# Performance work log

Measured on AMD Instinct MI355X. Metric: run time of the kernel, lower is better.

Reference implementation:

```python
import jax, jax.numpy as jnp
import numpy as np

N, D, E, K, L, NF, VOCAB = 100000, 128, 600000, 3, 3, 9, 100
BN_EPS = 1e-5
S = 0.05


def setup_inputs() -> dict:
    key = jax.random.key(0)
    ks = jax.random.split(key, 8)
    return {
        "x": jax.random.randint(ks[0], (N, NF), 0, VOCAB),
        "k_edges": jax.random.randint(ks[1], (K, 2, E), 0, N),
        "emb_tables": jax.random.normal(ks[2], (NF, VOCAB, D), jnp.float32) * S,
        "W1": jax.random.normal(ks[3], (L, D, 2 * D), jnp.float32) * S,
        "b1": jnp.zeros((L, 2 * D), jnp.float32),
        "g1": jnp.ones((L, 2 * D), jnp.float32),
        "be1": jnp.zeros((L, 2 * D), jnp.float32),
        "W2": jax.random.normal(ks[4], (L, 2 * D, D), jnp.float32) * S,
        "b2": jnp.zeros((L, D), jnp.float32),
        "eps": jnp.zeros((L,), jnp.float32),
        "alpha": jnp.zeros((L, K), jnp.float32),
        "bn_g": jnp.ones((L, D), jnp.float32),
        "bn_b": jnp.zeros((L, D), jnp.float32),
    }


def _bn(h, g, b):
    # training-mode BatchNorm1d over the node (batch) axis
    mu = h.mean(axis=0)
    var = h.var(axis=0)
    return (h - mu) * jax.lax.rsqrt(var + BN_EPS) * g + b


def _gin(h, src, dst, eps_l, W1_l, b1_l, g1_l, be1_l, W2_l, b2_l):
    # NodeGINConv (train_eps): mlp((1+eps)*x + sum_{j->i} x_j)
    agg = jax.ops.segment_sum(h[src], dst, num_segments=N)  # [N, D]
    z = (1.0 + eps_l) * h + agg
    z = jax.nn.relu(_bn(z @ W1_l + b1_l, g1_l, be1_l))  # [N, 2D]
    return z @ W2_l + b2_l  # [N, D]


def reference(x, k_edges, emb_tables, W1, b1, g1, be1, W2, b2, eps, alpha, bn_g, bn_b):
    # AtomEncoder: sum of per-feature embedding lookups -> [N, D]
    h = jnp.take_along_axis(
        emb_tables.transpose(1, 0, 2),  # [VOCAB, NF, D]
        x.T[..., None].transpose(1, 0, 2) * 0 + 0,  # placeholder avoided below
        axis=0,
    ) if False else emb_tables[jnp.arange(NF)[None, :], x].sum(axis=1)
    for l in range(L):
        # one shared wrapped GIN conv applied to each of the K relational edge sets
        msgs = jax.vmap(
            lambda e: _gin(h, e[0], e[1], eps[l], W1[l], b1[l], g1[l], be1[l], W2[l], b2[l])
        )(k_edges)  # [K, N, D]
        a = jax.nn.softmax(alpha[l])  # [K]
        h = jnp.einsum('knd,k->nd', msgs, a)
        h = jax.nn.relu(_bn(h, bn_g[l], bn_b[l]))  # dropout p=0 / eval -> identity
    return h
```

## Files before the change

kernel.cpp:

```cpp
#include <hip/hip_runtime.h>

#define NV     100000
#define DD     128
#define D2     256
#define EE     600000
#define KK     3
#define LL     3
#define NFEAT  9
#define VOCABS 100

#define NBKT   196
#define BCAP   8192

typedef __attribute__((ext_vector_type(8))) short short8;
typedef __attribute__((ext_vector_type(4))) float f32x4;
typedef __attribute__((ext_vector_type(2))) float f32x2;
typedef __attribute__((ext_vector_type(4))) unsigned int uint4v;

#define PA      0

#define ZS(k)  ((k)*512)
#define ZQ(k)  ((k)*512 + 256)
#define HSUM   1536
#define HSQ    1664

#define HB_OFF   ((size_t)0)
#define ZIN_OFF  ((size_t)25700000)
#define HNB_OFF  ((size_t)102500000)
#define O_BASE   ((size_t)128100000)


__device__ __forceinline__ unsigned short f2bf(float f) {
    union { float f; unsigned int u; } v; v.f = f;
    return (unsigned short)((v.u + 0x7FFFu + ((v.u >> 16) & 1u)) >> 16);
}
__device__ __forceinline__ float bf2f(unsigned short u) {
    union { unsigned int u; float f; } v; v.u = ((unsigned int)u) << 16;
    return v.f;
}
__device__ __forceinline__ f32x2 up2(unsigned int v) {
    union { unsigned int u[2]; f32x2 f; } w;
    w.u[0] = v << 16;
    w.u[1] = v & 0xFFFF0000u;
    return w.f;
}

__global__ void k_embed(const int* __restrict__ x, const float* __restrict__ emb,
                        unsigned short* __restrict__ hb) {
    int id = blockIdx.x*256 + threadIdx.x;
    int n = id >> 5, q = id & 31;
    if (n >= NV) {
        if (n < NV + 8) *(unsigned long long*)(hb + (size_t)n*DD + q*4) = 0ull;
        return;
    }
    const int* xr = x + n*NFEAT;
    f32x4 acc = {0.f,0.f,0.f,0.f};
    #pragma unroll
    for (int f = 0; f < NFEAT; ++f) {
        int idx = xr[f];
        acc += *(const f32x4*)(emb + ((size_t)(f*VOCABS + idx)*DD + q*4));
    }
    unsigned short pk[4];
    pk[0] = f2bf(acc[0]); pk[1] = f2bf(acc[1]); pk[2] = f2bf(acc[2]); pk[3] = f2bf(acc[3]);
    *(unsigned long long*)(hb + (size_t)n*DD + q*4) = *(unsigned long long*)pk;
}

__global__ void kA_bin(const int* __restrict__ ke, int* __restrict__ cursor,
                       uint2* __restrict__ pairs) {
    __shared__ int hist[NBKT], excl[NBKT], ofs[NBKT], gbase[NBKT];
    __shared__ int sc[256];
    __shared__ uint2 buf[4096];
    const int rel = blockIdx.y, t = threadIdx.x;
    const int e0 = blockIdx.x * 4096;
    const int cnt = min(4096, EE - e0);
    const int* srcA = ke + (size_t)(rel*2)*EE + e0;
    const int* dstA = ke + (size_t)(rel*2+1)*EE + e0;
    if (t < NBKT) hist[t] = 0;
    __syncthreads();
    for (int i = t; i < cnt; i += 256) atomicAdd(&hist[dstA[i] >> 9], 1);
    __syncthreads();
    const int hv = (t < NBKT) ? hist[t] : 0;
    sc[t] = hv;
    for (int off = 1; off < 256; off <<= 1) {
        __syncthreads();
        int v = (t >= off) ? sc[t-off] : 0;
        __syncthreads();
        sc[t] += v;
    }
    __syncthreads();
    if (t < NBKT) {
        excl[t] = sc[t] - hv;
        ofs[t]  = sc[t] - hv;
        if (hv > 0) gbase[t] = atomicAdd(&cursor[rel*NBKT + t], hv);
    }
    __syncthreads();
    for (int i = t; i < cnt; i += 256) {
        unsigned int s = (unsigned int)srcA[i], d = (unsigned int)dstA[i];
        int p = atomicAdd(&ofs[d >> 9], 1);
        uint2 u; u.x = s; u.y = d;
        buf[p] = u;
    }
    __syncthreads();
    for (int i = t; i < cnt; i += 256) {
        uint2 u = buf[i];
        int b = (int)(u.y >> 9);
        int pos = gbase[b] + (i - excl[b]);
        if (pos < BCAP) pairs[(size_t)(rel*NBKT + b)*BCAP + pos] = u;
    }
}

__global__ void kB_scan(const int* __restrict__ cursor, int* __restrict__ ebase) {
    __shared__ int sc[256];
    const int t = threadIdx.x;
    for (int rel = 0; rel < KK; ++rel) {
        int hv = (t < NBKT) ? min(cursor[rel*NBKT + t], BCAP) : 0;
        sc[t] = hv;
        for (int off = 1; off < 256; off <<= 1) {
            __syncthreads();
            int v = (t >= off) ? sc[t-off] : 0;
            __syncthreads();
            sc[t] += v;
        }
        __syncthreads();
        if (t < NBKT) ebase[rel*NBKT + t] = sc[t] - hv;
        __syncthreads();
    }
}

__global__ void kB_fill(const uint2* __restrict__ pairs, const int* __restrict__ cursor,
                        const int* __restrict__ ebase, int* __restrict__ rp,
                        int* __restrict__ col) {
    __shared__ int h2[512], excl[512], cur[512], sc[256];
    const int b = blockIdx.x, rel = blockIdx.y, t = threadIdx.x;
    const int lo = b * 512;
    const int cnt = min(cursor[rel*NBKT + b], BCAP);
    const int base = ebase[rel*NBKT + b];
    const uint2* P = pairs + (size_t)(rel*NBKT + b)*BCAP;
    h2[t] = 0; h2[t+256] = 0; cur[t] = 0; cur[t+256] = 0;
    __syncthreads();
    for (int i = t; i < cnt; i += 256) atomicAdd(&h2[(int)P[i].y - lo], 1);
    __syncthreads();
    const int a0 = h2[2*t], a1 = h2[2*t+1];
    sc[t] = a0 + a1;
    for (int off = 1; off < 256; off <<= 1) {
        __syncthreads();
        int v = (t >= off) ? sc[t-off] : 0;
        __syncthreads();
        sc[t] += v;
    }
    __syncthreads();
    const int e2 = sc[t] - (a0 + a1);
    excl[2*t] = e2; excl[2*t+1] = e2 + a0;
    __syncthreads();
    for (int tt = t; tt < 512; tt += 256) {
        int n = lo + tt;
        if (n <= NV) rp[(size_t)rel*(NV+1) + n] = base + excl[tt];
    }
    for (int i = t; i < cnt; i += 256) {
        uint2 u = P[i];
        int r = (int)u.y - lo;
        int p = atomicAdd(&cur[r], 1);
        col[(size_t)rel*EE + base + excl[r] + p] = (int)u.x;
    }
}

__global__ void k_prep(const float* __restrict__ W1, const float* __restrict__ W2,
                       const float* __restrict__ alpha, const int l,
                       unsigned short* __restrict__ w1f, unsigned short* __restrict__ w2f,
                       float* __restrict__ params) {
    int id = blockIdx.x*256 + threadIdx.x;
    if (id == 0) {
        float a0 = alpha[l*KK+0], a1 = alpha[l*KK+1], a2 = alpha[l*KK+2];
        float m = fmaxf(a0, fmaxf(a1, a2));
        float e0 = expf(a0-m), e1 = expf(a1-m), e2 = expf(a2-m);
        float inv = 1.f/(e0+e1+e2);
        params[PA+0] = e0*inv; params[PA+1] = e1*inv; params[PA+2] = e2*inv;
    }
    if (id < 4096) {
        int kt = id >> 10, nt = (id >> 6) & 15, lane = id & 63;
        int r = lane & 15, g = lane >> 4;
        const float* Wl = W1 + (size_t)l*DD*D2;
        #pragma unroll
        for (int e = 0; e < 8; ++e) {
            int kk = kt*32 + g*8 + e, c = nt*16 + r;
            w1f[(size_t)id*8 + e] = f2bf(Wl[(size_t)kk*D2 + c]);
        }
    } else if (id < 8192) {
        int id2 = id - 4096;
        int kt = id2 >> 9, nt = (id2 >> 6) & 7, lane = id2 & 63;
        int r = lane & 15, g = lane >> 4;
        const float* Wl = W2 + (size_t)l*D2*DD;
        #pragma unroll
        for (int e = 0; e < 8; ++e) {
            int kk = kt*32 + g*8 + e, c = nt*16 + r;
            w2f[(size_t)id2*8 + e] = f2bf(Wl[(size_t)kk*DD + c]);
        }
    }
}

__global__ void k_gather3(const unsigned short* __restrict__ hb, const int* __restrict__ rp,
                          const int* __restrict__ col, const float* __restrict__ epsp,
                          unsigned short* __restrict__ zin) {
    int gid = blockIdx.x*256 + threadIdx.x;
    int n0 = gid >> 6;
    if (n0 >= NV) return;
    const int n = __builtin_amdgcn_readfirstlane(n0);
    const int lane = threadIdx.x & 63;
    const int q = lane >> 4, r = lane & 15;
    const int r16 = r << 4;
    const char* hbase = (const char*)hb;
    const float epsv = 1.0f + epsp[0];
    const uint4v sv = *(const uint4v*)(hbase + (((unsigned)n << 8) + r16));
    int b0[KK], dg[KK], cv[KK];
    #pragma unroll
    for (int k = 0; k < KK; ++k) {
        int a = rp[k*(NV+1) + n];
        int b = rp[k*(NV+1) + n + 1];
        b0[k] = a; dg[k] = b - a;
        cv[k] = (lane < dg[k]) ? col[(size_t)k*EE + a + lane] : NV;
    }
    f32x2 acc[KK][4];
    #pragma unroll
    for (int k = 0; k < KK; ++k)
        #pragma unroll
        for (int c = 0; c < 4; ++c) acc[k][c] = (f32x2){0.f, 0.f};
    #pragma unroll
    for (int k = 0; k < KK; ++k) {
        const int dc = min(dg[k], 64);
        for (int base = 0; base < dc; base += 8) {
            int s0 = __shfl(cv[k], base + q);
            int s1 = __shfl(cv[k], base + q + 4);
            uint4v v0 = *(const uint4v*)(hbase + (((unsigned)s0 << 8) + r16));
            uint4v v1 = *(const uint4v*)(hbase + (((unsigned)s1 << 8) + r16));
            #pragma unroll
            for (int c = 0; c < 4; ++c) {
                acc[k][c] += up2(v0[c]);
                acc[k][c] += up2(v1[c]);
            }
        }
        for (int j = b0[k] + 64 + q; j < b0[k] + dg[k]; j += 4) {
            int s0 = col[(size_t)k*EE + j];
            uint4v v0 = *(const uint4v*)(hbase + (((unsigned)s0 << 8) + r16));
            #pragma unroll
            for (int c = 0; c < 4; ++c) acc[k][c] += up2(v0[c]);
        }
    }
    #pragma unroll
    for (int k = 0; k < KK; ++k) {
        #pragma unroll
        for (int c = 0; c < 4; ++c) {
            acc[k][c][0] += __shfl_xor(acc[k][c][0], 16);
            acc[k][c][1] += __shfl_xor(acc[k][c][1], 16);
            acc[k][c][0] += __shfl_xor(acc[k][c][0], 32);
            acc[k][c][1] += __shfl_xor(acc[k][c][1], 32);
        }
    }
    if (q == 0) {
        const unsigned dsto = (((unsigned)n >> 4) << 12) + ((unsigned)r << 8)
                            + (((unsigned)n & 15u) << 4);
        #pragma unroll
        for (int k = 0; k < KK; ++k) {
            uint4v pk;
            #pragma unroll
            for (int c = 0; c < 4; ++c) {
                f32x2 s2 = up2(sv[c]);
                float lo = acc[k][c][0] + epsv * s2[0];
                float hi = acc[k][c][1] + epsv * s2[1];
                unsigned int pko;
                asm("v_cvt_pk_bf16_f32 %0, %1, %2" : "=v"(pko) : "v"(lo), "v"(hi));
                pk[c] = pko;
            }
            *(uint4v*)((char*)zin + (size_t)k*NV*256 + dsto) = pk;
        }
    }
}

__launch_bounds__(256, 2)
__global__ void k_stats3(const unsigned short* __restrict__ zin,
                         const unsigned short* __restrict__ w1f,
                         float* __restrict__ statsL) {
    __shared__ __align__(16) unsigned short bfr1[32768];
    __shared__ float scf[1024];
    const int t = threadIdx.x;
    const int krel = blockIdx.y;
    const char* zk = (const char*)zin + (size_t)krel*NV*256;
    float* zsum = statsL + ZS(krel);
    float* zsq  = statsL + ZQ(krel);
    for (int i = t; i < 4096; i += 256)
        *(uint4v*)(bfr1 + i*8) = *(const uint4v*)(w1f + i*8);
    const int lane = t & 63, w = t >> 6;
    const int r_ = lane & 15, g = lane >> 4;
    const int rt = w & 1, ch = w >> 1;
    __syncthreads();
    float ssum[8] = {0,0,0,0,0,0,0,0};
    float ssq[8]  = {0,0,0,0,0,0,0,0};
    for (int tile = blockIdx.x; tile < NV/32; tile += gridDim.x) {
        short8 af[4];
        #pragma unroll
        for (int kt = 0; kt < 4; ++kt)
            af[kt] = *(const short8*)(zk + (size_t)(tile*2 + rt)*4096 + kt*1024 + lane*16);
        #pragma unroll
        for (int ct = 0; ct < 8; ++ct) {
            const int ntg = ch*8 + ct;
            f32x4 c = {0.f,0.f,0.f,0.f};
            #pragma unroll
            for (int kt = 0; kt < 4; ++kt) {
                short8 b = *(const short8*)(bfr1 + ((size_t)((kt*16 + ntg)*64 + lane))*8);
                c = __builtin_amdgcn_mfma_f32_16x16x32_bf16(af[kt], b, c, 0, 0, 0);
            }
            float s = c[0]+c[1]+c[2]+c[3];
            float q = c[0]*c[0]+c[1]*c[1]+c[2]*c[2]+c[3]*c[3];
            s += __shfl_xor(s, 16); q += __shfl_xor(q, 16);
            s += __shfl_xor(s, 32); q += __shfl_xor(q, 32);
            ssum[ct] += s; ssq[ct] += q;
        }
    }
    if (g == 0) {
        #pragma unroll
        for (int ct = 0; ct < 8; ++ct) {
            const int colc = (ch*8 + ct)*16 + r_;
            scf[rt*256 + colc]       = ssum[ct];
            scf[512 + rt*256 + colc] = ssq[ct];
        }
    }
    __syncthreads();
    atomicAdd(zsum + t, scf[t]       + scf[256 + t]);
    atomicAdd(zsq  + t, scf[512 + t] + scf[768 + t]);
}

__launch_bounds__(512, 2)
__global__ void k_gemm2f(const unsigned short* __restrict__ zin,
                         const unsigned short* __restrict__ w1f,
                         const unsigned short* __restrict__ w2f,
                         const float* __restrict__ g1l, const float* __restrict__ be1l,
                         const float* __restrict__ params,
                         float* __restrict__ statsL,
                         unsigned short* __restrict__ hnb) {
    __shared__ __align__(16) unsigned short bfr1[32768];
    __shared__ __align__(16) unsigned short bfr2[32768];
    __shared__ __align__(16) unsigned char yt[16384];
    const int t = threadIdx.x;
    for (int i = t; i < 4096; i += 512)
        *(uint4v*)(bfr1 + i*8) = *(const uint4v*)(w1f + i*8);
    for (int i = t; i < 4096; i += 512)
        *(uint4v*)(bfr2 + i*8) = *(const uint4v*)(w2f + i*8);
    const int lane = t & 63, w = t >> 6;
    const int r_ = lane & 15, g = lane >> 4;
    const int rt = w & 1, ch = w >> 1;
    const int arow = rt*16 + r_;
    float pa1[KK][4], pb1[KK][4];
    #pragma unroll
    for (int k = 0; k < KK; ++k) {
        const float ak = params[PA + k];
        #pragma unroll
        for (int ct = 0; ct < 4; ++ct) {
            const int colc = (ch*4 + ct)*16 + r_;
            float mu  = statsL[ZS(k) + colc] * (1.0f/NV);
            float var = statsL[ZQ(k) + colc] * (1.0f/NV) - mu*mu;
            float A = g1l[colc] * rsqrtf(var + 1e-5f);
            pa1[k][ct] = ak * A;
            pb1[k][ct] = ak * (be1l[colc] - mu*A);
        }
    }
    __syncthreads();
    float ssum[2] = {0,0}, ssq[2] = {0,0};
    for (int tile = blockIdx.x; tile < NV/32; tile += gridDim.x) {
        const int row0 = tile*32;
        f32x4 y[4];
        #pragma unroll
        for (int ct = 0; ct < 4; ++ct) y[ct] = (f32x4){0.f,0.f,0.f,0.f};
        short8 af[KK][4];
        #pragma unroll
        for (int k = 0; k < KK; ++k) {
            #pragma unroll
            for (int kt = 0; kt < 4; ++kt)
                af[k][kt] = *(const short8*)((const char*)zin + (size_t)k*NV*256
                              + (size_t)(tile*2 + rt)*4096 + kt*1024 + lane*16);
        }
        #pragma unroll
        for (int k = 0; k < KK; ++k) {
            #pragma unroll
            for (int ct = 0; ct < 4; ++ct) {
                const int ntg = ch*4 + ct;
                f32x4 c = {0.f,0.f,0.f,0.f};
                #pragma unroll
                for (int kt = 0; kt < 4; ++kt) {
                    short8 b = *(const short8*)(bfr1 + ((size_t)((kt*16 + ntg)*64 + lane))*8);
                    c = __builtin_amdgcn_mfma_f32_16x16x32_bf16(af[k][kt], b, c, 0, 0, 0);
                }
                #pragma unroll
                for (int reg = 0; reg < 4; ++reg)
                    y[ct][reg] += fmaxf(pa1[k][ct]*c[reg] + pb1[k][ct], 0.0f);
            }
        }
        __syncthreads();
        #pragma unroll
        for (int ct = 0; ct < 4; ++ct) {
            const int col2 = ((ch*4 + ct)*16 + r_)*2;
            #pragma unroll
            for (int reg = 0; reg < 4; ++reg) {
                const int row = rt*16 + g*4 + reg;
                *(unsigned short*)(yt + row*512 + (col2 ^ ((row & 15) << 4))) = f2bf(y[ct][reg]);
            }
        }
        __syncthreads();
        short8 ya[8];
        #pragma unroll
        for (int kt = 0; kt < 8; ++kt)
            ya[kt] = *(const short8*)(yt + arow*512 + ((kt*64 + g*16) ^ ((arow & 15) << 4)));
        #pragma unroll
        for (int ct2 = 0; ct2 < 2; ++ct2) {
            const int ntg2 = ch*2 + ct2;
            f32x4 c = {0.f,0.f,0.f,0.f};
            #pragma unroll
            for (int kt = 0; kt < 8; ++kt) {
                short8 b = *(const short8*)(bfr2 + ((size_t)((kt*8 + ntg2)*64 + lane))*8);
                c = __builtin_amdgcn_mfma_f32_16x16x32_bf16(ya[kt], b, c, 0, 0, 0);
            }
            unsigned short* hp = hnb + (size_t)(row0 + rt*16 + g*4)*DD + ntg2*16 + r_;
            float ps = 0.0f, pq = 0.0f;
            #pragma unroll
            for (int reg = 0; reg < 4; ++reg) {
                float xv = c[reg];
                hp[(size_t)reg*DD] = f2bf(xv);
                ps += xv; pq += xv*xv;
            }
            ps += __shfl_xor(ps, 16); pq += __shfl_xor(pq, 16);
            ps += __shfl_xor(ps, 32); pq += __shfl_xor(pq, 32);
            ssum[ct2] += ps; ssq[ct2] += pq;
        }
    }
    __syncthreads();
    float* scf = (float*)yt;
    if (g == 0) {
        #pragma unroll
        for (int ct2 = 0; ct2 < 2; ++ct2) {
            scf[w*32 + ct2*16 + r_]       = ssum[ct2];
            scf[256 + w*32 + ct2*16 + r_] = ssq[ct2];
        }
    }
    __syncthreads();
    if (t < 128) {
        const int chc = t >> 5, idx = t & 31;
        float s = 0.0f, q = 0.0f;
        #pragma unroll
        for (int rr = 0; rr < 2; ++rr) {
            s += scf[(chc*2 + rr)*32 + idx];
            q += scf[256 + (chc*2 + rr)*32 + idx];
        }
        atomicAdd(statsL + HSUM + t, s);
        atomicAdd(statsL + HSQ + t, q);
    }
}

__global__ void k_bnapply_mid(const unsigned short* __restrict__ hnb,
                              const float* __restrict__ statsL,
                              const float* __restrict__ bng, const float* __restrict__ bnb,
                              unsigned short* __restrict__ hb) {
    int id = blockIdx.x*256 + threadIdx.x;
    const int col0 = (id & 15)*8;
    short8 v = *(const short8*)(hnb + (size_t)id*8);
    short8 o;
    #pragma unroll
    for (int j = 0; j < 8; ++j) {
        const int c = col0 + j;
        float mu  = statsL[HSUM + c] * (1.0f/NV);
        float var = statsL[HSQ + c] * (1.0f/NV) - mu*mu;
        float A = bng[c] * rsqrtf(var + 1e-5f);
        float B = bnb[c] - mu*A;
        o[j] = (short)f2bf(fmaxf(A*bf2f((unsigned short)v[j]) + B, 0.0f));
    }
    *(short8*)(hb + (size_t)id*8) = o;
}

__global__ void k_bnapply_fin(const unsigned short* __restrict__ hnb,
                              const float* __restrict__ statsL,
                              const float* __restrict__ bng, const float* __restrict__ bnb,
                              float* __restrict__ out) {
    int id = blockIdx.x*256 + threadIdx.x;
    const int col0 = (id & 15)*8;
    short8 v = *(const short8*)(hnb + (size_t)id*8);
    f32x4 o0, o1;
    #pragma unroll
    for (int j = 0; j < 8; ++j) {
        const int c = col0 + j;
        float mu  = statsL[HSUM + c] * (1.0f/NV);
        float var = statsL[HSQ + c] * (1.0f/NV) - mu*mu;
        float A = bng[c] * rsqrtf(var + 1e-5f);
        float B = bnb[c] - mu*A;
        float r = fmaxf(A*bf2f((unsigned short)v[j]) + B, 0.0f);
        if (j < 4) o0[j] = r; else o1[j-4] = r;
    }
    *(f32x4*)(out + (size_t)id*8)     = o0;
    *(f32x4*)(out + (size_t)id*8 + 4) = o1;
}

extern "C" void kernel_launch(void* const* d_in, const int* in_sizes, int n_in,
                              void* d_out, int out_size, void* d_ws, size_t ws_size,
                              hipStream_t stream) {
    const int*   x     = (const int*)d_in[0];
    const int*   ke    = (const int*)d_in[1];
    const float* emb   = (const float*)d_in[2];
    const float* W1    = (const float*)d_in[3];
    const float* g1    = (const float*)d_in[5];
    const float* be1   = (const float*)d_in[6];
    const float* W2    = (const float*)d_in[7];
    const float* eps   = (const float*)d_in[9];
    const float* alpha = (const float*)d_in[10];
    const float* bng   = (const float*)d_in[11];
    const float* bnb   = (const float*)d_in[12];

    char* ws = (char*)d_ws;
    unsigned short* hb     = (unsigned short*)(ws + HB_OFF);
    unsigned short* zin    = (unsigned short*)(ws + ZIN_OFF);
    unsigned short* hnb    = (unsigned short*)(ws + HNB_OFF);
    size_t o = O_BASE;
    unsigned short* w1f    = (unsigned short*)(ws + o);          o += 65536;
    unsigned short* w2f    = (unsigned short*)(ws + o);          o += 65536;
    float*          stats  = (float*)(ws + o);                   o += 32768;
    float*          params = (float*)(ws + o);                   o += 4096;
    int*            rp     = (int*)(ws + o);                     o += 1200128;
    int*            col    = (int*)(ws + o);                     o += 7200000;
    int*            cur    = (int*)(ws + o);                     o += 4096;
    int*            ebase  = (int*)(ws + o);                     o += 4096;
    uint2*          pairs  = (uint2*)(ws + ZIN_OFF);

    k_embed<<<12501, 256, 0, stream>>>(x, emb, hb);

    hipMemsetAsync(cur, 0, KK*NBKT*sizeof(int), stream);
    hipMemsetAsync(stats, 0, 3*2048*sizeof(float), stream);
    kA_bin<<<dim3(147, KK), 256, 0, stream>>>(ke, cur, pairs);
    kB_scan<<<1, 256, 0, stream>>>(cur, ebase);
    kB_fill<<<dim3(NBKT, KK), 256, 0, stream>>>(pairs, cur, ebase, rp, col);

    for (int l = 0; l < LL; ++l) {
        float* statsL = stats + (size_t)l*2048;
        k_prep<<<32, 256, 0, stream>>>(W1, W2, alpha, l, w1f, w2f, params);
        k_gather3<<<25000, 256, 0, stream>>>(hb, rp, col, eps + l, zin);
        k_stats3<<<dim3(512, KK), 256, 0, stream>>>(zin, w1f, statsL);
        k_gemm2f<<<256, 512, 0, stream>>>(zin, w1f, w2f, g1 + l*D2, be1 + l*D2,
                                          params, statsL, hnb);
        if (l < LL-1) k_bnapply_mid<<<6250, 256, 0, stream>>>(hnb, statsL,
                                                              bng + l*DD, bnb + l*DD, hb);
        else          k_bnapply_fin<<<6250, 256, 0, stream>>>(hnb, statsL,
                                                              bng + l*DD, bnb + l*DD,
                                                              (float*)d_out);
    }
}
```

Measured before the change: 688.9 us.

## Pack edge pairs into 32-bit words, hoist weight prep, merge stats relations

Edge binning now packs the local destination offset and the source index into one 32-bit word instead of a uint2, so the pairs buffer traffic is halved. Each element's bucket is then found by binary search over the bucket prefix offsets rather than read from the pair. Weight conversion for all layers moves into a single launch before the layer loop, which removes one launch per layer. The stats kernel loops over the three relations inside one 256-block grid so each block loads W1 into shared memory once rather than once per relation. The packing assumes node ids fit in 17 bits, which holds for 100000 nodes.

New measurement: 653.4 us, median of 2. -5.2%, faster.

```diff
diff --git a/kernel.cpp b/kernel.cpp
--- a/kernel.cpp
+++ b/kernel.cpp
@@ -17,8 +17,6 @@
 typedef __attribute__((ext_vector_type(2))) float f32x2;
 typedef __attribute__((ext_vector_type(4))) unsigned int uint4v;
 
-#define PA      0
-
 #define ZS(k)  ((k)*512)
 #define ZQ(k)  ((k)*512 + 256)
 #define HSUM   1536
@@ -66,10 +64,10 @@
 }
 
 __global__ void kA_bin(const int* __restrict__ ke, int* __restrict__ cursor,
-                       uint2* __restrict__ pairs) {
+                       unsigned int* __restrict__ pairs) {
     __shared__ int hist[NBKT], excl[NBKT], ofs[NBKT], gbase[NBKT];
     __shared__ int sc[256];
-    __shared__ uint2 buf[4096];
+    __shared__ unsigned int buf[4096];
     const int rel = blockIdx.y, t = threadIdx.x;
     const int e0 = blockIdx.x * 4096;
     const int cnt = min(4096, EE - e0);
@@ -97,13 +95,20 @@
     for (int i = t; i < cnt; i += 256) {
         unsigned int s = (unsigned int)srcA[i], d = (unsigned int)dstA[i];
         int p = atomicAdd(&ofs[d >> 9], 1);
-        uint2 u; u.x = s; u.y = d;
-        buf[p] = u;
+        buf[p] = ((d & 511u) << 17) | s;
     }
     __syncthreads();
     for (int i = t; i < cnt; i += 256) {
-        uint2 u = buf[i];
-        int b = (int)(u.y >> 9);
+        unsigned int u = buf[i];
+        int lo = 0, hi = NBKT - 1;
+        #pragma unroll
+        for (int s2 = 0; s2 < 8; ++s2) {
+            int mid = (lo + hi + 1) >> 1;
+            bool ge = (i >= excl[mid]);
+            lo = ge ? mid : lo;
+            hi = ge ? hi : mid - 1;
+        }
+        const int b = lo;
         int pos = gbase[b] + (i - excl[b]);
         if (pos < BCAP) pairs[(size_t)(rel*NBKT + b)*BCAP + pos] = u;
     }
@@ -127,7 +132,7 @@
     }
 }
 
-__global__ void kB_fill(const uint2* __restrict__ pairs, const int* __restrict__ cursor,
+__global__ void kB_fill(const unsigned int* __restrict__ pairs, const int* __restrict__ cursor,
                         const int* __restrict__ ebase, int* __restrict__ rp,
                         int* __restrict__ col) {
     __shared__ int h2[512], excl[512], cur[512], sc[256];
@@ -135,10 +140,10 @@
     const int lo = b * 512;
     const int cnt = min(cursor[rel*NBKT + b], BCAP);
     const int base = ebase[rel*NBKT + b];
-    const uint2* P = pairs + (size_t)(rel*NBKT + b)*BCAP;
+    const unsigned int* P = pairs + (size_t)(rel*NBKT + b)*BCAP;
     h2[t] = 0; h2[t+256] = 0; cur[t] = 0; cur[t+256] = 0;
     __syncthreads();
-    for (int i = t; i < cnt; i += 256) atomicAdd(&h2[(int)P[i].y - lo], 1);
+    for (int i = t; i < cnt; i += 256) atomicAdd(&h2[P[i] >> 17], 1);
     __syncthreads();
     const int a0 = h2[2*t], a1 = h2[2*t+1];
     sc[t] = a0 + a1;
@@ -157,24 +162,25 @@
         if (n <= NV) rp[(size_t)rel*(NV+1) + n] = base + excl[tt];
     }
     for (int i = t; i < cnt; i += 256) {
-        uint2 u = P[i];
-        int r = (int)u.y - lo;
+        unsigned int u = P[i];
+        int r = (int)(u >> 17);
         int p = atomicAdd(&cur[r], 1);
-        col[(size_t)rel*EE + base + excl[r] + p] = (int)u.x;
-    }
-}
-
-__global__ void k_prep(const float* __restrict__ W1, const float* __restrict__ W2,
-                       const float* __restrict__ alpha, const int l,
-                       unsigned short* __restrict__ w1f, unsigned short* __restrict__ w2f,
-                       float* __restrict__ params) {
+        col[(size_t)rel*EE + base + excl[r] + p] = (int)(u & 0x1FFFFu);
+    }
+}
+
+__global__ void k_prep_all(const float* __restrict__ W1, const float* __restrict__ W2,
+                           const float* __restrict__ alpha,
+                           unsigned short* __restrict__ w1f, unsigned short* __restrict__ w2f,
+                           float* __restrict__ params) {
+    const int l = blockIdx.y;
     int id = blockIdx.x*256 + threadIdx.x;
     if (id == 0) {
         float a0 = alpha[l*KK+0], a1 = alpha[l*KK+1], a2 = alpha[l*KK+2];
         float m = fmaxf(a0, fmaxf(a1, a2));
         float e0 = expf(a0-m), e1 = expf(a1-m), e2 = expf(a2-m);
         float inv = 1.f/(e0+e1+e2);
-        params[PA+0] = e0*inv; params[PA+1] = e1*inv; params[PA+2] = e2*inv;
+        params[l*4+0] = e0*inv; params[l*4+1] = e1*inv; params[l*4+2] = e2*inv;
     }
     if (id < 4096) {
         int kt = id >> 10, nt = (id >> 6) & 15, lane = id & 63;
@@ -183,7 +189,7 @@
         #pragma unroll
         for (int e = 0; e < 8; ++e) {
             int kk = kt*32 + g*8 + e, c = nt*16 + r;
-            w1f[(size_t)id*8 + e] = f2bf(Wl[(size_t)kk*D2 + c]);
+            w1f[(size_t)l*32768 + (size_t)id*8 + e] = f2bf(Wl[(size_t)kk*D2 + c]);
         }
     } else if (id < 8192) {
         int id2 = id - 4096;
@@ -193,7 +199,7 @@
         #pragma unroll
         for (int e = 0; e < 8; ++e) {
             int kk = kt*32 + g*8 + e, c = nt*16 + r;
-            w2f[(size_t)id2*8 + e] = f2bf(Wl[(size_t)kk*DD + c]);
+            w2f[(size_t)l*32768 + (size_t)id2*8 + e] = f2bf(Wl[(size_t)kk*DD + c]);
         }
     }
 }
@@ -282,50 +288,50 @@
     __shared__ __align__(16) unsigned short bfr1[32768];
     __shared__ float scf[1024];
     const int t = threadIdx.x;
-    const int krel = blockIdx.y;
-    const char* zk = (const char*)zin + (size_t)krel*NV*256;
-    float* zsum = statsL + ZS(krel);
-    float* zsq  = statsL + ZQ(krel);
     for (int i = t; i < 4096; i += 256)
         *(uint4v*)(bfr1 + i*8) = *(const uint4v*)(w1f + i*8);
     const int lane = t & 63, w = t >> 6;
     const int r_ = lane & 15, g = lane >> 4;
     const int rt = w & 1, ch = w >> 1;
     __syncthreads();
-    float ssum[8] = {0,0,0,0,0,0,0,0};
-    float ssq[8]  = {0,0,0,0,0,0,0,0};
-    for (int tile = blockIdx.x; tile < NV/32; tile += gridDim.x) {
-        short8 af[4];
-        #pragma unroll
-        for (int kt = 0; kt < 4; ++kt)
-            af[kt] = *(const short8*)(zk + (size_t)(tile*2 + rt)*4096 + kt*1024 + lane*16);
-        #pragma unroll
-        for (int ct = 0; ct < 8; ++ct) {
-            const int ntg = ch*8 + ct;
-            f32x4 c = {0.f,0.f,0.f,0.f};
-            #pragma unroll
-            for (int kt = 0; kt < 4; ++kt) {
-                short8 b = *(const short8*)(bfr1 + ((size_t)((kt*16 + ntg)*64 + lane))*8);
-                c = __builtin_amdgcn_mfma_f32_16x16x32_bf16(af[kt], b, c, 0, 0, 0);
-            }
-            float s = c[0]+c[1]+c[2]+c[3];
-            float q = c[0]*c[0]+c[1]*c[1]+c[2]*c[2]+c[3]*c[3];
-            s += __shfl_xor(s, 16); q += __shfl_xor(q, 16);
-            s += __shfl_xor(s, 32); q += __shfl_xor(q, 32);
-            ssum[ct] += s; ssq[ct] += q;
-        }
-    }
-    if (g == 0) {
-        #pragma unroll
-        for (int ct = 0; ct < 8; ++ct) {
-            const int colc = (ch*8 + ct)*16 + r_;
-            scf[rt*256 + colc]       = ssum[ct];
-            scf[512 + rt*256 + colc] = ssq[ct];
-        }
-    }
-    __syncthreads();
-    atomicAdd(zsum + t, scf[t]       + scf[256 + t]);
-    atomicAdd(zsq  + t, scf[512 + t] + scf[768 + t]);
+    for (int krel = 0; krel < KK; ++krel) {
+        const char* zk = (const char*)zin + (size_t)krel*NV*256;
+        float ssum[8] = {0,0,0,0,0,0,0,0};
+        float ssq[8]  = {0,0,0,0,0,0,0,0};
+        for (int tile = blockIdx.x; tile < NV/32; tile += gridDim.x) {
+            short8 af[4];
+            #pragma unroll
+            for (int kt = 0; kt < 4; ++kt)
+                af[kt] = *(const short8*)(zk + (size_t)(tile*2 + rt)*4096 + kt*1024 + lane*16);
+            #pragma unroll
+            for (int ct = 0; ct < 8; ++ct) {
+                const int ntg = ch*8 + ct;
+                f32x4 c = {0.f,0.f,0.f,0.f};
+                #pragma unroll
+                for (int kt = 0; kt < 4; ++kt) {
+                    short8 b = *(const short8*)(bfr1 + ((size_t)((kt*16 + ntg)*64 + lane))*8);
+                    c = __builtin_amdgcn_mfma_f32_16x16x32_bf16(af[kt], b, c, 0, 0, 0);
+                }
+                float s = c[0]+c[1]+c[2]+c[3];
+                float q = c[0]*c[0]+c[1]*c[1]+c[2]*c[2]+c[3]*c[3];
+                s += __shfl_xor(s, 16); q += __shfl_xor(q, 16);
+                s += __shfl_xor(s, 32); q += __shfl_xor(q, 32);
+                ssum[ct] += s; ssq[ct] += q;
+            }
+        }
+        __syncthreads();
+        if (g == 0) {
+            #pragma unroll
+            for (int ct = 0; ct < 8; ++ct) {
+                const int colc = (ch*8 + ct)*16 + r_;
+                scf[rt*256 + colc]       = ssum[ct];
+                scf[512 + rt*256 + colc] = ssq[ct];
+            }
+        }
+        __syncthreads();
+        atomicAdd(statsL + ZS(krel) + t, scf[t]       + scf[256 + t]);
+        atomicAdd(statsL + ZQ(krel) + t, scf[512 + t] + scf[768 + t]);
+    }
 }
 
 __launch_bounds__(512, 2)
@@ -351,7 +357,7 @@
     float pa1[KK][4], pb1[KK][4];
     #pragma unroll
     for (int k = 0; k < KK; ++k) {
-        const float ak = params[PA + k];
+        const float ak = params[k];
         #pragma unroll
         for (int ct = 0; ct < 4; ++ct) {
             const int colc = (ch*4 + ct)*16 + r_;
@@ -515,17 +521,19 @@
     unsigned short* zin    = (unsigned short*)(ws + ZIN_OFF);
     unsigned short* hnb    = (unsigned short*)(ws + HNB_OFF);
     size_t o = O_BASE;
-    unsigned short* w1f    = (unsigned short*)(ws + o);          o += 65536;
-    unsigned short* w2f    = (unsigned short*)(ws + o);          o += 65536;
+    unsigned short* w1f    = (unsigned short*)(ws + o);          o += 3*65536;
+    unsigned short* w2f    = (unsigned short*)(ws + o);          o += 3*65536;
     float*          stats  = (float*)(ws + o);                   o += 32768;
     float*          params = (float*)(ws + o);                   o += 4096;
     int*            rp     = (int*)(ws + o);                     o += 1200128;
     int*            col    = (int*)(ws + o);                     o += 7200000;
     int*            cur    = (int*)(ws + o);                     o += 4096;
     int*            ebase  = (int*)(ws + o);                     o += 4096;
-    uint2*          pairs  = (uint2*)(ws + ZIN_OFF);
+    unsigned int*   pairs  = (unsigned int*)(ws + ZIN_OFF);
 
     k_embed<<<12501, 256, 0, stream>>>(x, emb, hb);
+
+    k_prep_all<<<dim3(32, LL), 256, 0, stream>>>(W1, W2, alpha, w1f, w2f, params);
 
     hipMemsetAsync(cur, 0, KK*NBKT*sizeof(int), stream);
     hipMemsetAsync(stats, 0, 3*2048*sizeof(float), stream);
@@ -535,11 +543,12 @@
 
     for (int l = 0; l < LL; ++l) {
         float* statsL = stats + (size_t)l*2048;
-        k_prep<<<32, 256, 0, stream>>>(W1, W2, alpha, l, w1f, w2f, params);
+        unsigned short* w1fl = w1f + (size_t)l*32768;
+        unsigned short* w2fl = w2f + (size_t)l*32768;
         k_gather3<<<25000, 256, 0, stream>>>(hb, rp, col, eps + l, zin);
-        k_stats3<<<dim3(512, KK), 256, 0, stream>>>(zin, w1f, statsL);
-        k_gemm2f<<<256, 512, 0, stream>>>(zin, w1f, w2f, g1 + l*D2, be1 + l*D2,
-                                          params, statsL, hnb);
+        k_stats3<<<256, 256, 0, stream>>>(zin, w1fl, statsL);
+        k_gemm2f<<<256, 512, 0, stream>>>(zin, w1fl, w2fl, g1 + l*D2, be1 + l*D2,
+                                          params + l*4, statsL, hnb);
         if (l < LL-1) k_bnapply_mid<<<6250, 256, 0, stream>>>(hnb, statsL,
                                                               bng + l*DD, bnb + l*DD, hb);
         else          k_bnapply_fin<<<6250, 256, 0, stream>>>(hnb, statsL,
```
